# Performance work log

Hardware: AMD Instinct MI355X
Metric: run time of the kernel (lower is better)

The kernel has to match this reference:

```python
import jax, jax.numpy as jnp
import numpy as np

B, L, S, E, D = 16, 2048, 2048, 64, 64

def setup_inputs() -> dict:
    key = jax.random.key(0)
    k1, k2, k3, k4 = jax.random.split(key, 4)
    queries = jax.random.normal(k1, (B, L, E), dtype=jnp.float32)
    keys = jax.random.normal(k2, (B, S, E), dtype=jnp.float32)
    values = jax.random.normal(k3, (B, S, D), dtype=jnp.float32)
    mlp = jax.random.normal(k4, (L, L), dtype=jnp.float32)  # learned seq-mix matrix
    return {"queries": queries, "keys": keys, "values": values, "mlp": mlp}

def reference(queries, keys, values, mlp):
    # scale = 1/sqrt(E) (self.scale is None)
    E_dim = queries.shape[-1]
    scale = 1.0 / jnp.sqrt(jnp.asarray(E_dim, dtype=queries.dtype))
    # scores: [B, L, S]
    scores = jnp.einsum('ble,bse->bls', queries, keys)
    # dropout omitted (eval mode / attention_dropout=0)
    A = jax.nn.softmax(scale * scores, axis=-1)
    # attention output: [B, L, D]
    V = jnp.einsum('bls,bsd->bld', A, values)
    # learned sequence-mixing: [B, L, D] -> [B, P, D] with P == L
    out = jnp.einsum('bld,pl->bpd', V, mlp)
    return out
```

## Files before the change

kernel.cpp:

```cpp
#include <hip/hip_runtime.h>

#define NB 16
#define NL 2048
#define NS 2048
#define NE 64
#define ND 64

typedef float floatx4 __attribute__((ext_vector_type(4)));
typedef _Float16 half8 __attribute__((ext_vector_type(8)));
typedef __fp16 half2v __attribute__((ext_vector_type(2)));

union H8 { half8 v; half2v h2[4]; };

__device__ __forceinline__ half8 cvt8(floatx4 a, floatx4 b) {
  H8 h;
  h.h2[0] = __builtin_amdgcn_cvt_pkrtz(a[0], a[1]);
  h.h2[1] = __builtin_amdgcn_cvt_pkrtz(a[2], a[3]);
  h.h2[2] = __builtin_amdgcn_cvt_pkrtz(b[0], b[1]);
  h.h2[3] = __builtin_amdgcn_cvt_pkrtz(b[2], b[3]);
  return h.v;
}

__device__ __forceinline__ void async16(void* l, const void* g) {
  __builtin_amdgcn_global_load_lds((__attribute__((address_space(1))) void*)g,
                                   (__attribute__((address_space(3))) void*)l, 16, 0, 0);
}

#define B1_WAIT8  { asm volatile("s_waitcnt vmcnt(8)" ::: "memory"); __builtin_amdgcn_s_barrier(); }
#define B1_WAIT0  { asm volatile("s_waitcnt vmcnt(0)" ::: "memory"); __builtin_amdgcn_s_barrier(); }
#define B2_LGKM   { asm volatile("s_waitcnt lgkmcnt(0)" ::: "memory"); __builtin_amdgcn_s_barrier(); }

__device__ __forceinline__ int kinv(int y) {
  return (y & 0x23) | ((y & 8) << 1) | ((y & 4) << 1) | ((y & 16) >> 2);
}

__global__ __launch_bounds__(256) void prep_k(const float* __restrict__ V,
                                              const float* __restrict__ K,
                                              _Float16* __restrict__ Vt,
                                              _Float16* __restrict__ Kh,
                                              int do_k) {
  __shared__ __align__(16) _Float16 Vl[64][72];
  const int bid = blockIdx.x;
  const int t = threadIdx.x;

  if (bid < 512) {
    const int b = bid >> 5;
    const int s0 = (bid & 31) * 64;
    {
      int sl = t & 63;
      int dg = t >> 6;
      const float* src = V + ((size_t)(b * NS + s0 + sl)) * ND + dg * 16;
      int x = kinv(sl);
      #pragma unroll
      for (int c = 0; c < 4; ++c) {
        floatx4 v = *(const floatx4*)(src + c * 4);
        #pragma unroll
        for (int e = 0; e < 4; ++e) Vl[dg * 16 + c * 4 + e][x] = (_Float16)v[e];
      }
    }
    __syncthreads();
    {
      int d = t & 63;
      int xg = t >> 6;
      int dk = (d & 7) << 3;
      #pragma unroll
      for (int h = 0; h < 2; ++h) {
        int x = xg * 16 + h * 8;
        half8 v = *(const half8*)&Vl[d][x];
        *(half8*)(Vt + ((size_t)(b * ND + d)) * NS + s0 + (x ^ dk)) = v;
      }
    }
  } else {
    if (!do_k) return;
    int c = (bid - 512) * 256 + t;
    int j = c & 7;
    int s = (c >> 3) & (NS - 1);
    int b = c >> 14;
    const float* src = K + ((size_t)(b * NS + s)) * NE + j * 8;
    half8 h = cvt8(*(const floatx4*)src, *(const floatx4*)(src + 4));
    *(half8*)(Kh + ((size_t)(b * NS + s)) * NE + (j ^ (s & 7)) * 8) = h;
  }
}

template<bool KH16>
__global__ __launch_bounds__(512) void attn_k(const float* __restrict__ Q,
                                              const void* __restrict__ Ksrc,
                                              const _Float16* __restrict__ Vtp,
                                              _Float16* __restrict__ Vatt,
                                              const float* __restrict__ Mf,
                                              _Float16* __restrict__ Mh) {
  __shared__ __align__(16) char smem[100352];
  const int tid = threadIdx.x;
  const int wid = tid >> 6, lane = tid & 63;
  const int lr = lane & 15, lg = lane >> 4;
  const int g = wid & 3;
  const int qh = wid >> 2;
  const int L = blockIdx.y * 16 + blockIdx.x;
  const int b = (L & 7) * 2 + ((L >> 3) & 1);
  const int qx = L >> 4;
  const int qbase = qx * 128 + qh * 64;
  const _Float16* Kh = (const _Float16*)Ksrc;
  const float* Kf = (const float*)Ksrc;

  constexpr float SC = 0.18033688f;
  half8 qf[4][2];
  #pragma unroll
  for (int sub = 0; sub < 4; ++sub)
    #pragma unroll
    for (int kk = 0; kk < 2; ++kk) {
      const float* qp = Q + ((size_t)(b * NL + qbase + sub * 16 + lr)) * NE + kk * 32 + lg * 8;
      floatx4 a = *(const floatx4*)qp, c = *(const floatx4*)(qp + 4);
      qf[sub][kk] = cvt8(a * SC, c * SC);
    }

  half8 ones;
  #pragma unroll
  for (int i = 0; i < 8; ++i) ones[i] = (_Float16)1.0f;

  floatx4 oacc[4][4], lacc[4];
  #pragma unroll
  for (int s = 0; s < 4; ++s) {
    lacc[s] = (floatx4){0.f, 0.f, 0.f, 0.f};
    #pragma unroll
    for (int m = 0; m < 4; ++m) oacc[s][m] = (floatx4){0.f, 0.f, 0.f, 0.f};
  }

  int kOff[2][2], vOff[4];
  #pragma unroll
  for (int mt = 0; mt < 2; ++mt)
    #pragma unroll
    for (int kk = 0; kk < 2; ++kk) {
      int row = g * 32 + mt * 16 + lr, col = kk * 32 + lg * 8;
      kOff[mt][kk] = (row * 128 + col * 2) ^ ((row & 7) << 4);
    }
  #pragma unroll
  for (int mt = 0; mt < 4; ++mt) {
    int row = mt * 16 + lr;
    vOff[mt] = row * 256 + (g >> 1) * 128 + (((g & 1) * 64 + lg * 16) ^ ((row & 7) << 4));
  }

  auto stageV = [&](int buf, int s0) {
    #pragma unroll
    for (int i = 0; i < 2; ++i) {
      int co = (wid * 2 + i) * 1024;
      int o = co + lane * 16;
      int row = o >> 8, c16 = (o >> 4) & 15;
      async16(smem + 49152 + buf * 16384 + co,
              Vtp + ((size_t)(b * ND + row)) * NS + s0 + c16 * 8);
    }
  };
  auto stageK = [&](int buf, int s0) {
    if constexpr (KH16) {
      #pragma unroll
      for (int i = 0; i < 2; ++i) {
        int co = (wid * 2 + i) * 1024;
        int o = co + lane * 16;
        int row = o >> 7, c8 = (o >> 4) & 7;
        async16(smem + buf * 16384 + co,
                Kh + ((size_t)(b * NS + s0 + row)) * NE + c8 * 8);
      }
    } else {
      int row = tid >> 2, cg = (tid & 3) * 16;
      const float* kp = Kf + ((size_t)(b * NS + s0 + row)) * NE + cg;
      #pragma unroll
      for (int c = 0; c < 2; ++c) {
        half8 h = cvt8(*(const floatx4*)(kp + c * 8), *(const floatx4*)(kp + c * 8 + 4));
        int col = cg + c * 8;
        *(half8*)(smem + buf * 16384 + ((row * 128 + col * 2) ^ ((row & 7) << 4))) = h;
      }
    }
  };

  stageK(0, 0); stageV(0, 0);

  int br = 0;
  for (int t = 0; t < NS / 128; ++t) {
    int bn = (br == 2) ? 0 : br + 1;
    if (t + 1 < NS / 128) {
      stageK(bn, (t + 1) * 128); stageV(bn, (t + 1) * 128);
      if constexpr (KH16) {
        asm volatile("s_waitcnt vmcnt(4)" ::: "memory");
        __builtin_amdgcn_s_barrier();
      } else __syncthreads();
    } else {
      if constexpr (KH16) {
        asm volatile("s_waitcnt vmcnt(0)" ::: "memory");
        __builtin_amdgcn_s_barrier();
      } else __syncthreads();
    }

    const char* kb = smem + br * 16384;
    const char* vb = smem + 49152 + br * 16384;

    half8 kf[2][2];
    #pragma unroll
    for (int mt = 0; mt < 2; ++mt)
      #pragma unroll
      for (int kk = 0; kk < 2; ++kk)
        kf[mt][kk] = *(const half8*)(kb + kOff[mt][kk]);

    H8 bf[4];
    #pragma unroll
    for (int sub = 0; sub < 4; ++sub) {
      floatx4 sacc[2];
      #pragma unroll
      for (int mt = 0; mt < 2; ++mt) sacc[mt] = (floatx4){0.f, 0.f, 0.f, 0.f};
      __builtin_amdgcn_s_setprio(1);
      #pragma unroll
      for (int kk = 0; kk < 2; ++kk)
        #pragma unroll
        for (int mt = 0; mt < 2; ++mt)
          sacc[mt] = __builtin_amdgcn_mfma_f32_16x16x32_f16(kf[mt][kk], qf[sub][kk], sacc[mt], 0, 0, 0);
      __builtin_amdgcn_s_setprio(0);

      float p00 = __builtin_amdgcn_exp2f(sacc[0][0]);
      float p01 = __builtin_amdgcn_exp2f(sacc[0][1]);
      float p02 = __builtin_amdgcn_exp2f(sacc[0][2]);
      float p03 = __builtin_amdgcn_exp2f(sacc[0][3]);
      float p10 = __builtin_amdgcn_exp2f(sacc[1][0]);
      float p11 = __builtin_amdgcn_exp2f(sacc[1][1]);
      float p12 = __builtin_amdgcn_exp2f(sacc[1][2]);
      float p13 = __builtin_amdgcn_exp2f(sacc[1][3]);
      bf[sub].h2[0] = __builtin_amdgcn_cvt_pkrtz(p00, p01);
      bf[sub].h2[1] = __builtin_amdgcn_cvt_pkrtz(p02, p03);
      bf[sub].h2[2] = __builtin_amdgcn_cvt_pkrtz(p10, p11);
      bf[sub].h2[3] = __builtin_amdgcn_cvt_pkrtz(p12, p13);
    }

    __builtin_amdgcn_s_setprio(1);
    #pragma unroll
    for (int mt = 0; mt < 4; ++mt) {
      half8 vt = *(const half8*)(vb + vOff[mt]);
      #pragma unroll
      for (int sub = 0; sub < 4; ++sub)
        oacc[sub][mt] = __builtin_amdgcn_mfma_f32_16x16x32_f16(vt, bf[sub].v, oacc[sub][mt], 0, 0, 0);
    }
    #pragma unroll
    for (int sub = 0; sub < 4; ++sub)
      lacc[sub] = __builtin_amdgcn_mfma_f32_16x16x32_f16(ones, bf[sub].v, lacc[sub], 0, 0, 0);
    __builtin_amdgcn_s_setprio(0);
    br = bn;
  }

  __syncthreads();

  {
    char* red = smem + qh * 49152;
    char* lred = smem + 98304 + qh * 768;
    if (g != 0) {
      #pragma unroll
      for (int sub = 0; sub < 4; ++sub)
        #pragma unroll
        for (int mt = 0; mt < 4; ++mt) {
          int idx = sub * 4 + mt;
          *(floatx4*)(red + (g - 1) * 16384 + lane * 256 + ((idx ^ (lane & 15)) * 16)) = oacc[sub][mt];
        }
      if (lg == 0) {
        #pragma unroll
        for (int sub = 0; sub < 4; ++sub)
          *(float*)(lred + (g - 1) * 256 + lr * 16 + sub * 4) = lacc[sub][0];
      }
    }
    __syncthreads();
    if (g == 0) {
      #pragma unroll
      for (int sub = 0; sub < 4; ++sub) {
        float lt = lacc[sub][0];
        #pragma unroll
        for (int gg = 0; gg < 3; ++gg)
          lt += *(const float*)(lred + gg * 256 + lr * 16 + sub * 4);
        float inv = __builtin_amdgcn_rcpf(lt);
        int l = qbase + sub * 16 + lr;
        #pragma unroll
        for (int mt = 0; mt < 4; ++mt) {
          floatx4 o = oacc[sub][mt];
          int idx = sub * 4 + mt;
          #pragma unroll
          for (int gg = 0; gg < 3; ++gg)
            o += *(const floatx4*)(red + gg * 16384 + lane * 256 + ((idx ^ (lane & 15)) * 16));
          #pragma unroll
          for (int r = 0; r < 4; ++r) {
            int d = mt * 16 + lg * 4 + r;
            int lsw = (l & ~63) | ((l & 63) ^ ((d & 7) << 3));
            Vatt[((size_t)(b * ND + d)) * NL + lsw] = (_Float16)(o[r] * inv);
          }
        }
      }
    }
  }

  if constexpr (KH16) {
    int mb = blockIdx.y * 16 + blockIdx.x;
    #pragma unroll
    for (int q = 0; q < 4; ++q) {
      int c = mb * 2048 + q * 512 + tid;
      int j = c & 255, p = c >> 8;
      const float* src = Mf + (size_t)p * NL + j * 8;
      half8 h = cvt8(*(const floatx4*)src, *(const floatx4*)(src + 4));
      int jo = (j & ~7) | ((j & 7) ^ (p & 7));
      *(half8*)(Mh + (size_t)p * NL + jo * 8) = h;
    }
  }
}

template<bool A16>
__global__ __launch_bounds__(256) void mix_k(const void* __restrict__ Asrc,
                                             const _Float16* __restrict__ Bsrc,
                                             float* __restrict__ out) {
  __shared__ __align__(16) char smem[65536];
  const int tid = threadIdx.x;
  const int wid = tid >> 6, lane = tid & 63;
  const int lr = lane & 15, lg = lane >> 4;
  const int kh = wid & 1;
  const int mw = wid >> 1;
  const int L = blockIdx.y * 32 + blockIdx.x;
  const int i = L >> 3;
  const int p0 = ((L & 7) * 4 + (i & 3)) * 64;
  const int b = i >> 2;
  const _Float16* Ah = (const _Float16*)Asrc;
  const float* Af = (const float*)Asrc;

  floatx4 acc[2][4];
  #pragma unroll
  for (int mt = 0; mt < 2; ++mt)
    #pragma unroll
    for (int nt = 0; nt < 4; ++nt) acc[mt][nt] = (floatx4){0.f, 0.f, 0.f, 0.f};

  auto stage = [&](int buf, int t) {
    int k0 = kh * (NL / 2) + t * 64;
    if constexpr (A16) {
      #pragma unroll
      for (int i2 = 0; i2 < 4; ++i2) {
        int co = (mw * 4 + i2) * 1024;
        int o = co + lane * 16;
        int row = o >> 7, c8 = (o >> 4) & 7;
        async16(smem + kh * 16384 + buf * 8192 + co,
                Ah + ((size_t)(p0 + row)) * NL + k0 + c8 * 8);
      }
    } else {
      int row = (lane & 31) + mw * 32, cg = (lane >> 5) * 32;
      const float* ap = Af + ((size_t)(p0 + row)) * NL + k0 + cg;
      #pragma unroll
      for (int c = 0; c < 4; ++c) {
        half8 h = cvt8(*(const floatx4*)(ap + c * 8), *(const floatx4*)(ap + c * 8 + 4));
        int col = cg + c * 8;
        *(half8*)(smem + kh * 16384 + buf * 8192 +
                  ((row * 128 + col * 2) ^ ((row & 7) << 4))) = h;
      }
    }
    #pragma unroll
    for (int i2 = 0; i2 < 4; ++i2) {
      int co = (mw * 4 + i2) * 1024;
      int o = co + lane * 16;
      int row = o >> 7, c8 = (o >> 4) & 7;
      async16(smem + 32768 + kh * 16384 + buf * 8192 + co,
              Bsrc + ((size_t)(b * ND + row)) * NL + k0 + c8 * 8);
    }
  };

  stage(0, 0);
  if constexpr (!A16) __syncthreads();

  for (int t = 0; t < 16; ++t) {
    int buf = t & 1;
    if (t + 1 < 16) {
      stage(buf ^ 1, t + 1);
      if constexpr (A16) B1_WAIT8 else __syncthreads();
    } else {
      if constexpr (A16) B1_WAIT0
    }
    const char* ab = smem + kh * 16384 + buf * 8192;
    const char* bb = smem + 32768 + kh * 16384 + buf * 8192;
    #pragma unroll
    for (int kk = 0; kk < 2; ++kk) {
      int col = kk * 32 + lg * 8;
      half8 af[2];
      #pragma unroll
      for (int mt = 0; mt < 2; ++mt) {
        int row = mw * 32 + mt * 16 + lr;
        af[mt] = *(const half8*)(ab + ((row * 128 + col * 2) ^ ((row & 7) << 4)));
      }
      __builtin_amdgcn_s_setprio(1);
      #pragma unroll
      for (int nt = 0; nt < 4; ++nt) {
        int row = nt * 16 + lr;
        half8 bfr = *(const half8*)(bb + ((row * 128 + col * 2) ^ ((row & 7) << 4)));
        #pragma unroll
        for (int mt = 0; mt < 2; ++mt)
          acc[mt][nt] = __builtin_amdgcn_mfma_f32_16x16x32_f16(af[mt], bfr, acc[mt][nt], 0, 0, 0);
      }
      __builtin_amdgcn_s_setprio(0);
    }
    if constexpr (A16) B2_LGKM else __syncthreads();
  }

  if (kh == 1) {
    #pragma unroll
    for (int mt = 0; mt < 2; ++mt)
      #pragma unroll
      for (int nt = 0; nt < 4; ++nt) {
        int idx = mt * 4 + nt;
        *(floatx4*)(smem + mw * 8192 + lane * 128 + ((idx ^ (lane & 7)) * 16)) = acc[mt][nt];
      }
  }
  __syncthreads();
  if (kh == 0) {
    #pragma unroll
    for (int mt = 0; mt < 2; ++mt)
      #pragma unroll
      for (int nt = 0; nt < 4; ++nt) {
        int idx = mt * 4 + nt;
        acc[mt][nt] += *(const floatx4*)(smem + mw * 8192 + lane * 128 + ((idx ^ (lane & 7)) * 16));
        #pragma unroll
        for (int r = 0; r < 4; ++r) {
          int p = p0 + mw * 32 + mt * 16 + lg * 4 + r;
          int d = nt * 16 + lr;
          out[((size_t)(b * NL + p)) * ND + d] = acc[mt][nt][r];
        }
      }
  }
}

extern "C" void kernel_launch(void* const* d_in, const int* in_sizes, int n_in,
                              void* d_out, int out_size, void* d_ws, size_t ws_size,
                              hipStream_t stream) {
  (void)in_sizes; (void)n_in; (void)out_size;
  const float* Q = (const float*)d_in[0];
  const float* K = (const float*)d_in[1];
  const float* V = (const float*)d_in[2];
  const float* M = (const float*)d_in[3];
  float* out = (float*)d_out;

  char* ws = (char*)d_ws;
  _Float16* Vtp  = (_Float16*)ws;
  _Float16* Vatt = (_Float16*)(ws + (4u << 20));
  _Float16* Kh   = (_Float16*)(ws + (8u << 20));
  _Float16* Mh   = (_Float16*)(ws + (12u << 20));
  bool big = ws_size >= (size_t)(20u << 20);

  if (big) {
    prep_k<<<1536, 256, 0, stream>>>(V, K, Vtp, Kh, 1);
    attn_k<true><<<dim3(16, 16), 512, 0, stream>>>(Q, Kh, Vtp, Vatt, M, Mh);
    mix_k<true><<<dim3(32, 16), 256, 0, stream>>>(Mh, Vatt, out);
  } else {
    prep_k<<<512, 256, 0, stream>>>(V, K, Vtp, Kh, 0);
    attn_k<false><<<dim3(16, 16), 512, 0, stream>>>(Q, K, Vtp, Vatt, nullptr, nullptr);
    mix_k<false><<<dim3(32, 16), 256, 0, stream>>>(M, Vatt, out);
  }
}
```

Measured before the change: 54.56 us.

## Halve attention query tile per block and switch to double-buffered K/V staging

New measurement: 53.60 us. Within noise of the previous version (-1.8%).

```diff
diff --git a/kernel.cpp b/kernel.cpp
--- a/kernel.cpp
+++ b/kernel.cpp
@@ -83,29 +83,29 @@
 }
 
 template<bool KH16>
-__global__ __launch_bounds__(512) void attn_k(const float* __restrict__ Q,
-                                              const void* __restrict__ Ksrc,
-                                              const _Float16* __restrict__ Vtp,
-                                              _Float16* __restrict__ Vatt,
-                                              const float* __restrict__ Mf,
-                                              _Float16* __restrict__ Mh) {
-  __shared__ __align__(16) char smem[100352];
+__global__ __launch_bounds__(512, 4) void attn_k(const float* __restrict__ Q,
+                                                 const void* __restrict__ Ksrc,
+                                                 const _Float16* __restrict__ Vtp,
+                                                 _Float16* __restrict__ Vatt,
+                                                 const float* __restrict__ Mf,
+                                                 _Float16* __restrict__ Mh) {
+  __shared__ __align__(16) char smem[65536];
   const int tid = threadIdx.x;
   const int wid = tid >> 6, lane = tid & 63;
   const int lr = lane & 15, lg = lane >> 4;
   const int g = wid & 3;
   const int qh = wid >> 2;
-  const int L = blockIdx.y * 16 + blockIdx.x;
+  const int L = blockIdx.y * 32 + blockIdx.x;
   const int b = (L & 7) * 2 + ((L >> 3) & 1);
   const int qx = L >> 4;
-  const int qbase = qx * 128 + qh * 64;
+  const int qbase = qx * 64 + qh * 32;
   const _Float16* Kh = (const _Float16*)Ksrc;
   const float* Kf = (const float*)Ksrc;
 
   constexpr float SC = 0.18033688f;
-  half8 qf[4][2];
-  #pragma unroll
-  for (int sub = 0; sub < 4; ++sub)
+  half8 qf[2][2];
+  #pragma unroll
+  for (int sub = 0; sub < 2; ++sub)
     #pragma unroll
     for (int kk = 0; kk < 2; ++kk) {
       const float* qp = Q + ((size_t)(b * NL + qbase + sub * 16 + lr)) * NE + kk * 32 + lg * 8;
@@ -117,9 +117,9 @@
   #pragma unroll
   for (int i = 0; i < 8; ++i) ones[i] = (_Float16)1.0f;
 
-  floatx4 oacc[4][4], lacc[4];
-  #pragma unroll
-  for (int s = 0; s < 4; ++s) {
+  floatx4 oacc[2][4], lacc[2];
+  #pragma unroll
+  for (int s = 0; s < 2; ++s) {
     lacc[s] = (floatx4){0.f, 0.f, 0.f, 0.f};
     #pragma unroll
     for (int m = 0; m < 4; ++m) oacc[s][m] = (floatx4){0.f, 0.f, 0.f, 0.f};
@@ -145,7 +145,7 @@
       int co = (wid * 2 + i) * 1024;
       int o = co + lane * 16;
       int row = o >> 8, c16 = (o >> 4) & 15;
-      async16(smem + 49152 + buf * 16384 + co,
+      async16(smem + 32768 + buf * 16384 + co,
               Vtp + ((size_t)(b * ND + row)) * NS + s0 + c16 * 8);
     }
   };
@@ -173,44 +173,31 @@
 
   stageK(0, 0); stageV(0, 0);
 
-  int br = 0;
   for (int t = 0; t < NS / 128; ++t) {
-    int bn = (br == 2) ? 0 : br + 1;
-    if (t + 1 < NS / 128) {
-      stageK(bn, (t + 1) * 128); stageV(bn, (t + 1) * 128);
-      if constexpr (KH16) {
-        asm volatile("s_waitcnt vmcnt(4)" ::: "memory");
-        __builtin_amdgcn_s_barrier();
-      } else __syncthreads();
-    } else {
-      if constexpr (KH16) {
-        asm volatile("s_waitcnt vmcnt(0)" ::: "memory");
-        __builtin_amdgcn_s_barrier();
-      } else __syncthreads();
-    }
-
-    const char* kb = smem + br * 16384;
-    const char* vb = smem + 49152 + br * 16384;
-
-    half8 kf[2][2];
-    #pragma unroll
-    for (int mt = 0; mt < 2; ++mt)
-      #pragma unroll
-      for (int kk = 0; kk < 2; ++kk)
-        kf[mt][kk] = *(const half8*)(kb + kOff[mt][kk]);
-
-    H8 bf[4];
-    #pragma unroll
-    for (int sub = 0; sub < 4; ++sub) {
+    int buf = t & 1;
+    if constexpr (KH16) {
+      asm volatile("s_waitcnt vmcnt(0)" ::: "memory");
+      __builtin_amdgcn_s_barrier();
+    } else __syncthreads();
+    if (t + 1 < NS / 128) { stageK(buf ^ 1, (t + 1) * 128); stageV(buf ^ 1, (t + 1) * 128); }
+
+    const char* kb = smem + buf * 16384;
+    const char* vb = smem + 32768 + buf * 16384;
+
+    H8 bf[2];
+    #pragma unroll
+    for (int sub = 0; sub < 2; ++sub) {
       floatx4 sacc[2];
       #pragma unroll
       for (int mt = 0; mt < 2; ++mt) sacc[mt] = (floatx4){0.f, 0.f, 0.f, 0.f};
       __builtin_amdgcn_s_setprio(1);
       #pragma unroll
-      for (int kk = 0; kk < 2; ++kk)
-        #pragma unroll
-        for (int mt = 0; mt < 2; ++mt)
-          sacc[mt] = __builtin_amdgcn_mfma_f32_16x16x32_f16(kf[mt][kk], qf[sub][kk], sacc[mt], 0, 0, 0);
+      for (int kk = 0; kk < 2; ++kk) {
+        half8 kf0 = *(const half8*)(kb + kOff[0][kk]);
+        half8 kf1 = *(const half8*)(kb + kOff[1][kk]);
+        sacc[0] = __builtin_amdgcn_mfma_f32_16x16x32_f16(kf0, qf[sub][kk], sacc[0], 0, 0, 0);
+        sacc[1] = __builtin_amdgcn_mfma_f32_16x16x32_f16(kf1, qf[sub][kk], sacc[1], 0, 0, 0);
+      }
       __builtin_amdgcn_s_setprio(0);
 
       float p00 = __builtin_amdgcn_exp2f(sacc[0][0]);
@@ -231,44 +218,40 @@
     #pragma unroll
     for (int mt = 0; mt < 4; ++mt) {
       half8 vt = *(const half8*)(vb + vOff[mt]);
-      #pragma unroll
-      for (int sub = 0; sub < 4; ++sub)
-        oacc[sub][mt] = __builtin_amdgcn_mfma_f32_16x16x32_f16(vt, bf[sub].v, oacc[sub][mt], 0, 0, 0);
-    }
-    #pragma unroll
-    for (int sub = 0; sub < 4; ++sub)
-      lacc[sub] = __builtin_amdgcn_mfma_f32_16x16x32_f16(ones, bf[sub].v, lacc[sub], 0, 0, 0);
+      oacc[0][mt] = __builtin_amdgcn_mfma_f32_16x16x32_f16(vt, bf[0].v, oacc[0][mt], 0, 0, 0);
+      oacc[1][mt] = __builtin_amdgcn_mfma_f32_16x16x32_f16(vt, bf[1].v, oacc[1][mt], 0, 0, 0);
+    }
+    lacc[0] = __builtin_amdgcn_mfma_f32_16x16x32_f16(ones, bf[0].v, lacc[0], 0, 0, 0);
+    lacc[1] = __builtin_amdgcn_mfma_f32_16x16x32_f16(ones, bf[1].v, lacc[1], 0, 0, 0);
     __builtin_amdgcn_s_setprio(0);
-    br = bn;
   }
 
   __syncthreads();
 
   {
-    char* red = smem + qh * 49152;
-    char* lred = smem + 98304 + qh * 768;
+    char* red = smem + qh * 24576;
+    char* lann = smem + 49152 + qh * 768;
     if (g != 0) {
       #pragma unroll
-      for (int sub = 0; sub < 4; ++sub)
+      for (int sub = 0; sub < 2; ++sub)
         #pragma unroll
         for (int mt = 0; mt < 4; ++mt) {
           int idx = sub * 4 + mt;
-          *(floatx4*)(red + (g - 1) * 16384 + lane * 256 + ((idx ^ (lane & 15)) * 16)) = oacc[sub][mt];
+          *(floatx4*)(red + (g - 1) * 8192 + lane * 128 + ((idx ^ (lane & 7)) * 16)) = oacc[sub][mt];
         }
       if (lg == 0) {
-        #pragma unroll
-        for (int sub = 0; sub < 4; ++sub)
-          *(float*)(lred + (g - 1) * 256 + lr * 16 + sub * 4) = lacc[sub][0];
+        *(float*)(lann + (g - 1) * 256 + lr * 16) = lacc[0][0];
+        *(float*)(lann + (g - 1) * 256 + lr * 16 + 4) = lacc[1][0];
       }
     }
     __syncthreads();
     if (g == 0) {
       #pragma unroll
-      for (int sub = 0; sub < 4; ++sub) {
+      for (int sub = 0; sub < 2; ++sub) {
         float lt = lacc[sub][0];
         #pragma unroll
         for (int gg = 0; gg < 3; ++gg)
-          lt += *(const float*)(lred + gg * 256 + lr * 16 + sub * 4);
+          lt += *(const float*)(lann + gg * 256 + lr * 16 + sub * 4);
         float inv = __builtin_amdgcn_rcpf(lt);
         int l = qbase + sub * 16 + lr;
         #pragma unroll
@@ -277,7 +260,7 @@
           int idx = sub * 4 + mt;
           #pragma unroll
           for (int gg = 0; gg < 3; ++gg)
-            o += *(const floatx4*)(red + gg * 16384 + lane * 256 + ((idx ^ (lane & 15)) * 16));
+            o += *(const floatx4*)(red + gg * 8192 + lane * 128 + ((idx ^ (lane & 7)) * 16));
           #pragma unroll
           for (int r = 0; r < 4; ++r) {
             int d = mt * 16 + lg * 4 + r;
@@ -290,10 +273,10 @@
   }
 
   if constexpr (KH16) {
-    int mb = blockIdx.y * 16 + blockIdx.x;
-    #pragma unroll
-    for (int q = 0; q < 4; ++q) {
-      int c = mb * 2048 + q * 512 + tid;
+    int mb = blockIdx.y * 32 + blockIdx.x;
+    #pragma unroll
+    for (int q = 0; q < 2; ++q) {
+      int c = mb * 1024 + q * 512 + tid;
       int j = c & 255, p = c >> 8;
       const float* src = Mf + (size_t)p * NL + j * 8;
       half8 h = cvt8(*(const floatx4*)src, *(const floatx4*)(src + 4));
@@ -440,11 +423,11 @@
 
   if (big) {
     prep_k<<<1536, 256, 0, stream>>>(V, K, Vtp, Kh, 1);
-    attn_k<true><<<dim3(16, 16), 512, 0, stream>>>(Q, Kh, Vtp, Vatt, M, Mh);
+    attn_k<true><<<dim3(32, 16), 512, 0, stream>>>(Q, Kh, Vtp, Vatt, M, Mh);
     mix_k<true><<<dim3(32, 16), 256, 0, stream>>>(Mh, Vatt, out);
   } else {
     prep_k<<<512, 256, 0, stream>>>(V, K, Vtp, Kh, 0);
-    attn_k<false><<<dim3(16, 16), 512, 0, stream>>>(Q, K, Vtp, Vatt, nullptr, nullptr);
+    attn_k<false><<<dim3(32, 16), 512, 0, stream>>>(Q, K, Vtp, Vatt, nullptr, nullptr);
     mix_k<false><<<dim3(32, 16), 256, 0, stream>>>(M, Vatt, out);
   }
 }
```
